# Kernel optimization log

Hardware: AMD Instinct MI355X
Metric: run time of the kernel (lower is better)

The kernel has to match this reference:

```python
import jax, jax.numpy as jnp
import numpy as np

# Quantum circuit closed form: per wire i, state |0> -> RX(x_i) -> RY(theta_i),
# then <PauliZ_i> = cos(theta_i) * cos(x_i). No entangling gates, so wires are
# independent and the whole per-token loop collapses to one elementwise op.

B, S, E = 8, 4096, 512
NQ, FFN = 8, 2048

def setup_inputs() -> dict:
    key = jax.random.key(0)
    ks = jax.random.split(key, 6)
    return {
        "x": jax.random.normal(ks[0], (B, S, E), dtype=jnp.float32),
        "theta": jax.random.normal(ks[1], (NQ,), dtype=jnp.float32),
        "W1": jax.random.normal(ks[2], (FFN, NQ), dtype=jnp.float32) * (1.0 / np.sqrt(NQ)),
        "b1": jax.random.normal(ks[3], (FFN,), dtype=jnp.float32) * 0.01,
        "W2": jax.random.normal(ks[4], (E, FFN), dtype=jnp.float32) * (1.0 / np.sqrt(FFN)),
        "b2": jax.random.normal(ks[5], (E,), dtype=jnp.float32) * 0.01,
    }

def reference(x, theta, W1, b1, W2, b2):
    n_qubits = theta.shape[0]
    # token_slice = x[:, :, :n_qubits]; <Z> = cos(theta) * cos(x)
    q_out = jnp.cos(x[..., :n_qubits]) * jnp.cos(theta)        # [B, S, NQ]
    h = jax.nn.relu(jnp.einsum('bsq,fq->bsf', q_out, W1) + b1)  # [B, S, FFN]
    out = jnp.einsum('bsf,ef->bse', h, W2) + b2                 # [B, S, E]
    return out
```

## Files before the change

### kernel.cpp

```cpp
#include <hip/hip_runtime.h>
#include <math.h>

typedef __attribute__((ext_vector_type(8)))  short short8;
typedef __attribute__((ext_vector_type(4)))  short short4_t;
typedef __attribute__((ext_vector_type(16))) float float16_t;

__device__ __forceinline__ short f2bf(float f) {
    union { float f; unsigned u; } c; c.f = f;
    unsigned u = c.u + 0x7fffu + ((c.u >> 16) & 1u);
    return (short)(u >> 16);
}
__device__ __forceinline__ float16_t zero16() {
    float16_t z;
#pragma unroll
    for (int r = 0; r < 16; ++r) z[r] = 0.0f;
    return z;
}

__global__ __launch_bounds__(256) void prep_kernel(
    const float* __restrict__ x, const float* __restrict__ theta,
    const float* __restrict__ W1, const float* __restrict__ W2,
    short* __restrict__ W2P, short* __restrict__ Qz, short* __restrict__ W1z)
{
    int gid = blockIdx.x * 256 + threadIdx.x;
    if (gid < 131072) {
        int lane = gid & 63;
        int ks   = (gid >> 6) & 127;
        int nt   = gid >> 13;
        int n = nt * 32 + (lane & 31);
        int k = ks * 16 + (lane >> 5) * 8;
        const float4* p = (const float4*)(W2 + n * 2048 + k);
        float4 v0 = p[0], v1 = p[1];
        short8 o;
        o[0] = f2bf(v0.x); o[1] = f2bf(v0.y); o[2] = f2bf(v0.z); o[3] = f2bf(v0.w);
        o[4] = f2bf(v1.x); o[5] = f2bf(v1.y); o[6] = f2bf(v1.z); o[7] = f2bf(v1.w);
        *(short8*)(W2P + gid * 8) = o;
    } else if (gid < 131072 + 32768) {
        int t = gid - 131072;
        const float4* xp = (const float4*)(x + t * 512);
        float4 x0 = xp[0], x1 = xp[1];
        float xv[8] = {x0.x, x0.y, x0.z, x0.w, x1.x, x1.y, x1.z, x1.w};
        short8 q;
#pragma unroll
        for (int c = 0; c < 8; ++c)
            q[c] = f2bf(cosf(xv[c]) * cosf(theta[c]));
        *(short8*)(Qz + t * 8) = q;
    } else if (gid < 131072 + 32768 + 2048) {
        int f = gid - (131072 + 32768);
        const float4* wp = (const float4*)(W1 + f * 8);
        float4 w0 = wp[0], w1 = wp[1];
        short8 wv;
        wv[0] = f2bf(w0.x); wv[1] = f2bf(w0.y); wv[2] = f2bf(w0.z); wv[3] = f2bf(w0.w);
        wv[4] = f2bf(w1.x); wv[5] = f2bf(w1.y); wv[6] = f2bf(w1.z); wv[7] = f2bf(w1.w);
        short8 z = {0,0,0,0,0,0,0,0};
        *(short8*)(W1z + f * 16) = wv;
        *(short8*)(W1z + f * 16 + 8) = z;
    }
}

__device__ __forceinline__ void stage1_tile(
    const short* __restrict__ W1z, const float* __restrict__ b1,
    short* __restrict__ dst, const short8* qf,
    int k0, int wx, int wy, int lh, int l31)
{
    short8 a1 = *(const short8*)(W1z + (k0 + wx * 32 + l31) * 16 + lh * 8);
    float4 bsv[4];
#pragma unroll
    for (int g = 0; g < 4; ++g)
        bsv[g] = *(const float4*)(b1 + k0 + wx * 32 + 4 * lh + 8 * g);
#pragma unroll
    for (int i = 0; i < 2; ++i) {
        float16_t d1 = __builtin_amdgcn_mfma_f32_32x32x16_bf16(
            a1, qf[i], zero16(), 0, 0, 0);
        const int m = wy * 64 + i * 32 + l31;
#pragma unroll
        for (int g = 0; g < 4; ++g) {
            float bb[4] = {bsv[g].x, bsv[g].y, bsv[g].z, bsv[g].w};
            short4_t p;
#pragma unroll
            for (int r = 0; r < 4; ++r) {
                float h = d1[g * 4 + r] + bb[r];
                h = fmaxf(h, 0.0f);
                p[r] = f2bf(h);
            }
            *(short4_t*)(dst + (wx * 4 + g) * 1024 + m * 8 + 4 * lh) = p;
        }
    }
}

__global__ __launch_bounds__(256, 2) void ffn_kernel(
    const short* __restrict__ Qz, const short* __restrict__ W1z,
    const short* __restrict__ W2P, const float* __restrict__ b1,
    const float* __restrict__ b2, float* __restrict__ out)
{
    __shared__ short Hs[2 * 8192];

    const int tid  = threadIdx.x;
    const int lane = tid & 63;
    const int w    = tid >> 6;
    const int wy = w & 1, wx = w >> 1;
    const int l31 = lane & 31, lh = lane >> 5;
    const int bid = blockIdx.x;
    const int nt = bid & 1, mt = bid >> 1;
    const int m0 = mt * 128, n0 = nt * 256;

    short8 qf[2];
#pragma unroll
    for (int i = 0; i < 2; ++i) {
        short8 v = {0,0,0,0,0,0,0,0};
        if (lh == 0)
            v = *(const short8*)(Qz + (m0 + wy * 64 + i * 32 + l31) * 8);
        qf[i] = v;
    }

    float16_t acc[2][4];
#pragma unroll
    for (int i = 0; i < 2; ++i)
#pragma unroll
        for (int j = 0; j < 4; ++j) acc[i][j] = zero16();

    stage1_tile(W1z, b1, Hs, qf, 0, wx, wy, lh, l31);
    __syncthreads();

    for (int kt = 0; kt < 32; ++kt) {
        const int p = kt & 1;
        const short* rd = Hs + p * 8192;

        if (kt < 31)
            stage1_tile(W1z, b1, Hs + (p ^ 1) * 8192, qf,
                        (kt + 1) * 64, wx, wy, lh, l31);

#pragma unroll
        for (int ks = 0; ks < 4; ++ks) {
            short8 bf[4];
#pragma unroll
            for (int j = 0; j < 4; ++j)
                bf[j] = *(const short8*)(W2P +
                    (((nt * 8 + wx * 4 + j) * 128 + (kt * 4 + ks)) * 64 + lane) * 8);
            short8 af[2];
#pragma unroll
            for (int i = 0; i < 2; ++i)
                af[i] = *(const short8*)(rd + (ks * 2 + lh) * 1024 +
                                         (wy * 64 + i * 32 + l31) * 8);
#pragma unroll
            for (int i = 0; i < 2; ++i)
#pragma unroll
                for (int j = 0; j < 4; ++j)
                    acc[i][j] = __builtin_amdgcn_mfma_f32_32x32x16_bf16(
                        af[i], bf[j], acc[i][j], 0, 0, 0);
        }
        __syncthreads();
    }

#pragma unroll
    for (int j = 0; j < 4; ++j) {
        const int n = n0 + wx * 128 + j * 32 + l31;
        const float b2v = b2[n];
#pragma unroll
        for (int i = 0; i < 2; ++i) {
            const int mbase = m0 + wy * 64 + i * 32 + 4 * lh;
#pragma unroll
            for (int r = 0; r < 16; ++r) {
                const int row = mbase + (r & 3) + 8 * (r >> 2);
                out[row * 512 + n] = acc[i][j][r] + b2v;
            }
        }
    }
}

extern "C" void kernel_launch(void* const* d_in, const int* in_sizes, int n_in,
                              void* d_out, int out_size, void* d_ws, size_t ws_size,
                              hipStream_t stream)
{
    const float* x     = (const float*)d_in[0];
    const float* theta = (const float*)d_in[1];
    const float* W1    = (const float*)d_in[2];
    const float* b1    = (const float*)d_in[3];
    const float* W2    = (const float*)d_in[4];
    const float* b2    = (const float*)d_in[5];
    float* out = (float*)d_out;

    short* W2P = (short*)d_ws;
    short* Qz  = (short*)((char*)d_ws + 2097152);
    short* W1z = (short*)((char*)d_ws + 2621440);

    prep_kernel<<<648, 256, 0, stream>>>(x, theta, W1, W2, W2P, Qz, W1z);
    ffn_kernel<<<512, 256, 0, stream>>>(Qz, W1z, W2P, b1, b2, out);
}
```

Before: 186.2 us.

## Fold b1 into stage-1 MFMA, prefetch W2 fragments, and truncate bf16 packing

The b1 bias is folded into the first GEMM by placing bf16(b1) in the zero-padded K half of W1z and a constant 1.0 in the matching Q fragment lane, so the per-tile bias loads and adds go away. All 16 W2 fragments for a k-tile are now loaded before the stage-1 compute so global latency overlaps with it. H is converted to bf16 by truncation with a byte permute instead of round-to-nearest. This raises register pressure and changes rounding of both b1 and H, which may slightly alter accuracy.

Result: faster. 173.8 us (-6.7%).

```diff
diff --git a/kernel.cpp b/kernel.cpp
--- a/kernel.cpp
+++ b/kernel.cpp
@@ -2,7 +2,6 @@
 #include <math.h>
 
 typedef __attribute__((ext_vector_type(8)))  short short8;
-typedef __attribute__((ext_vector_type(4)))  short short4_t;
 typedef __attribute__((ext_vector_type(16))) float float16_t;
 
 __device__ __forceinline__ short f2bf(float f) {
@@ -10,6 +9,9 @@
     unsigned u = c.u + 0x7fffu + ((c.u >> 16) & 1u);
     return (short)(u >> 16);
 }
+__device__ __forceinline__ unsigned fbits(float f) {
+    union { float f; unsigned u; } c; c.f = f; return c.u;
+}
 __device__ __forceinline__ float16_t zero16() {
     float16_t z;
 #pragma unroll
@@ -19,7 +21,8 @@
 
 __global__ __launch_bounds__(256) void prep_kernel(
     const float* __restrict__ x, const float* __restrict__ theta,
-    const float* __restrict__ W1, const float* __restrict__ W2,
+    const float* __restrict__ W1, const float* __restrict__ b1,
+    const float* __restrict__ W2,
     short* __restrict__ W2P, short* __restrict__ Qz, short* __restrict__ W1z)
 {
     int gid = blockIdx.x * 256 + threadIdx.x;
@@ -52,22 +55,17 @@
         short8 wv;
         wv[0] = f2bf(w0.x); wv[1] = f2bf(w0.y); wv[2] = f2bf(w0.z); wv[3] = f2bf(w0.w);
         wv[4] = f2bf(w1.x); wv[5] = f2bf(w1.y); wv[6] = f2bf(w1.z); wv[7] = f2bf(w1.w);
-        short8 z = {0,0,0,0,0,0,0,0};
+        short8 bz = {0,0,0,0,0,0,0,0};
+        bz[0] = f2bf(b1[f]);
         *(short8*)(W1z + f * 16) = wv;
-        *(short8*)(W1z + f * 16 + 8) = z;
+        *(short8*)(W1z + f * 16 + 8) = bz;
     }
 }
 
 __device__ __forceinline__ void stage1_tile(
-    const short* __restrict__ W1z, const float* __restrict__ b1,
-    short* __restrict__ dst, const short8* qf,
-    int k0, int wx, int wy, int lh, int l31)
-{
-    short8 a1 = *(const short8*)(W1z + (k0 + wx * 32 + l31) * 16 + lh * 8);
-    float4 bsv[4];
-#pragma unroll
-    for (int g = 0; g < 4; ++g)
-        bsv[g] = *(const float4*)(b1 + k0 + wx * 32 + 4 * lh + 8 * g);
+    short8 a1, const short8* qf, short* __restrict__ dst,
+    int wx, int wy, int lh, int l31)
+{
 #pragma unroll
     for (int i = 0; i < 2; ++i) {
         float16_t d1 = __builtin_amdgcn_mfma_f32_32x32x16_bf16(
@@ -75,23 +73,22 @@
         const int m = wy * 64 + i * 32 + l31;
 #pragma unroll
         for (int g = 0; g < 4; ++g) {
-            float bb[4] = {bsv[g].x, bsv[g].y, bsv[g].z, bsv[g].w};
-            short4_t p;
-#pragma unroll
-            for (int r = 0; r < 4; ++r) {
-                float h = d1[g * 4 + r] + bb[r];
-                h = fmaxf(h, 0.0f);
-                p[r] = f2bf(h);
-            }
-            *(short4_t*)(dst + (wx * 4 + g) * 1024 + m * 8 + 4 * lh) = p;
+            float v0 = fmaxf(d1[g * 4 + 0], 0.0f);
+            float v1 = fmaxf(d1[g * 4 + 1], 0.0f);
+            float v2 = fmaxf(d1[g * 4 + 2], 0.0f);
+            float v3 = fmaxf(d1[g * 4 + 3], 0.0f);
+            uint2 pp;
+            pp.x = __builtin_amdgcn_perm(fbits(v1), fbits(v0), 0x07060302u);
+            pp.y = __builtin_amdgcn_perm(fbits(v3), fbits(v2), 0x07060302u);
+            *(uint2*)(dst + (wx * 4 + g) * 1024 + m * 8 + 4 * lh) = pp;
         }
     }
 }
 
 __global__ __launch_bounds__(256, 2) void ffn_kernel(
     const short* __restrict__ Qz, const short* __restrict__ W1z,
-    const short* __restrict__ W2P, const float* __restrict__ b1,
-    const float* __restrict__ b2, float* __restrict__ out)
+    const short* __restrict__ W2P, const float* __restrict__ b2,
+    float* __restrict__ out)
 {
     __shared__ short Hs[2 * 8192];
 
@@ -110,33 +107,48 @@
         short8 v = {0,0,0,0,0,0,0,0};
         if (lh == 0)
             v = *(const short8*)(Qz + (m0 + wy * 64 + i * 32 + l31) * 8);
+        else
+            v[0] = (short)0x3F80;
         qf[i] = v;
     }
 
+    int w2base[4];
+#pragma unroll
+    for (int j = 0; j < 4; ++j)
+        w2base[j] = (nt * 8 + wx * 4 + j) * 65536 + lane * 8;
+
     float16_t acc[2][4];
 #pragma unroll
     for (int i = 0; i < 2; ++i)
 #pragma unroll
         for (int j = 0; j < 4; ++j) acc[i][j] = zero16();
 
-    stage1_tile(W1z, b1, Hs, qf, 0, wx, wy, lh, l31);
+    {
+        short8 a1 = *(const short8*)(W1z + (wx * 32 + l31) * 16 + lh * 8);
+        stage1_tile(a1, qf, Hs, wx, wy, lh, l31);
+    }
     __syncthreads();
 
     for (int kt = 0; kt < 32; ++kt) {
         const int p = kt & 1;
+
+        short8 a1 = {0,0,0,0,0,0,0,0};
+        if (kt < 31)
+            a1 = *(const short8*)(W1z + ((kt + 1) * 64 + wx * 32 + l31) * 16 + lh * 8);
+
+        short8 bfv[4][4];
+#pragma unroll
+        for (int ks = 0; ks < 4; ++ks)
+#pragma unroll
+            for (int j = 0; j < 4; ++j)
+                bfv[ks][j] = *(const short8*)(W2P + w2base[j] + (kt * 4 + ks) * 512);
+
+        if (kt < 31)
+            stage1_tile(a1, qf, Hs + (p ^ 1) * 8192, wx, wy, lh, l31);
+
         const short* rd = Hs + p * 8192;
-
-        if (kt < 31)
-            stage1_tile(W1z, b1, Hs + (p ^ 1) * 8192, qf,
-                        (kt + 1) * 64, wx, wy, lh, l31);
-
 #pragma unroll
         for (int ks = 0; ks < 4; ++ks) {
-            short8 bf[4];
-#pragma unroll
-            for (int j = 0; j < 4; ++j)
-                bf[j] = *(const short8*)(W2P +
-                    (((nt * 8 + wx * 4 + j) * 128 + (kt * 4 + ks)) * 64 + lane) * 8);
             short8 af[2];
 #pragma unroll
             for (int i = 0; i < 2; ++i)
@@ -147,7 +159,7 @@
 #pragma unroll
                 for (int j = 0; j < 4; ++j)
                     acc[i][j] = __builtin_amdgcn_mfma_f32_32x32x16_bf16(
-                        af[i], bf[j], acc[i][j], 0, 0, 0);
+                        af[i], bfv[ks][j], acc[i][j], 0, 0, 0);
         }
         __syncthreads();
     }
@@ -158,11 +170,11 @@
         const float b2v = b2[n];
 #pragma unroll
         for (int i = 0; i < 2; ++i) {
-            const int mbase = m0 + wy * 64 + i * 32 + 4 * lh;
+            const int base = (m0 + wy * 64 + i * 32 + 4 * lh) * 512 + n;
 #pragma unroll
             for (int r = 0; r < 16; ++r) {
-                const int row = mbase + (r & 3) + 8 * (r >> 2);
-                out[row * 512 + n] = acc[i][j][r] + b2v;
+                const int off = ((r & 3) + 8 * (r >> 2)) * 512;
+                out[base + off] = acc[i][j][r] + b2v;
             }
         }
     }
@@ -184,6 +196,6 @@
     short* Qz  = (short*)((char*)d_ws + 2097152);
     short* W1z = (short*)((char*)d_ws + 2621440);
 
-    prep_kernel<<<648, 256, 0, stream>>>(x, theta, W1, W2, W2P, Qz, W1z);
-    ffn_kernel<<<512, 256, 0, stream>>>(Qz, W1z, W2P, b1, b2, out);
-}
+    prep_kernel<<<648, 256, 0, stream>>>(x, theta, W1, b1, W2, W2P, Qz, W1z);
+    ffn_kernel<<<512, 256, 0, stream>>>(Qz, W1z, W2P, b2, out);
+}
```
